# Optimization experiments

Measured on AMD Instinct MI355X. Metric: run time of the kernel, lower is better.

The kernel has to match this reference:

```python
import jax, jax.numpy as jnp
import numpy as np

ALPHA = 0.2      # LeakyReLU negative slope
EPS = 1e-5       # LayerNorm eps
NEG = -9e15


def setup_inputs() -> dict:
    key = jax.random.key(0)
    ks = jax.random.split(key, 7)
    B, N, F_in, F_out = 8, 1024, 512, 512
    h1 = jax.random.normal(ks[0], (B, N, F_in), jnp.float32)
    h2 = jax.random.normal(ks[1], (B, N, F_in), jnp.float32)
    adj = jax.random.randint(ks[2], (B, N, N), 0, 2, jnp.int32)
    s = 1.414 * (6.0 / (F_in + F_out)) ** 0.5  # xavier_uniform gain=1.414
    W1 = jax.random.uniform(ks[3], (F_in, F_out), jnp.float32, -s, s)
    W2 = jax.random.uniform(ks[4], (F_in, F_out), jnp.float32, -s, s)
    W3 = jax.random.uniform(ks[5], (F_in, F_out), jnp.float32, -s, s)
    sa = 1.414 * (6.0 / (2 * F_out + 1)) ** 0.5
    a = jax.random.uniform(ks[6], (2 * F_out, 1), jnp.float32, -sa, sa)
    gamma = jnp.ones((F_out,), jnp.float32)
    beta = jnp.zeros((F_out,), jnp.float32)
    return {"h1": h1, "h2": h2, "adj": adj, "W1": W1, "W2": W2,
            "W3": W3, "a": a, "gamma": gamma, "beta": beta}


def reference(h1, h2, adj, W1, W2, W3, a, gamma, beta):
    F_out = W1.shape[1]
    Wh = h1 @ W1                      # [B,N,F]
    Wt = h2 @ W2                      # [B,N,F]
    a1 = a[:F_out, 0]                 # [F]
    a2 = a[F_out:, 0]                 # [F]
    # decomposed edge score: cat([Wh_i, Wt_j]) @ a == Wh_i@a1 + Wt_j@a2
    e = (Wh @ a1)[:, :, None] + (Wt @ a2)[:, None, :]   # [B,N,N]
    e = jnp.where(e > 0, e, ALPHA * e)                  # LeakyReLU
    e = jnp.where(adj > 0, e, NEG)
    attention = jax.nn.softmax(e, axis=2)               # [B,N,N]
    Wv = h2 @ W3                                        # [B,N,F]
    h_prime = attention @ Wv                            # [B,N,F]
    mu = jnp.mean(h_prime, axis=-1, keepdims=True)
    var = jnp.mean(jnp.square(h_prime - mu), axis=-1, keepdims=True)
    h_prime = (h_prime - mu) * jax.lax.rsqrt(var + EPS) * gamma + beta
    return jax.nn.gelu(h_prime, approximate=False)
```

## Files before the change

### kernel.cpp

```cpp
#include <hip/hip_runtime.h>
#include <math.h>

#define ALPHA 0.2f
#define NEGV  -9000000000000000.0f
#define EPSV  1e-5f

static constexpr int Bn = 8;
static constexpr int Nn = 1024;
static constexpr int Fn = 512;
static constexpr int M  = Bn * Nn;

typedef __attribute__((ext_vector_type(8))) short bf16x8;
typedef __attribute__((ext_vector_type(4))) float f32x4;

__device__ inline float wave_reduce_sum(float v) {
#pragma unroll
    for (int off = 32; off; off >>= 1) v += __shfl_xor(v, off);
    return v;
}
__device__ inline float wave_reduce_max(float v) {
#pragma unroll
    for (int off = 32; off; off >>= 1) v = fmaxf(v, __shfl_xor(v, off));
    return v;
}

__device__ inline unsigned short bf16_rne(float f) {
    union { float f; unsigned int u; } v; v.f = f;
    unsigned int r = v.u + 0x7FFFu + ((v.u >> 16) & 1u);
    return (unsigned short)(r >> 16);
}
__device__ inline float bf16_to_f(unsigned short h) {
    union { unsigned int u; float f; } v; v.u = (unsigned int)h << 16;
    return v.f;
}

__global__ __launch_bounds__(256) void k_pack(const int* __restrict__ adj,
                                              unsigned int* __restrict__ pk) {
    int idx = blockIdx.x * 256 + threadIdx.x;
    const int* p = adj + (size_t)idx * 32;
    unsigned int m = 0;
#pragma unroll
    for (int q = 0; q < 8; ++q) {
        int4 v = *(const int4*)&p[q * 4];
        m |= (unsigned)(v.x > 0) << (q * 4 + 0);
        m |= (unsigned)(v.y > 0) << (q * 4 + 1);
        m |= (unsigned)(v.z > 0) << (q * 4 + 2);
        m |= (unsigned)(v.w > 0) << (q * 4 + 3);
    }
    pk[idx] = m;
}

__global__ __launch_bounds__(64) void k_proj_w(const float* __restrict__ W1,
                                               const float* __restrict__ W2,
                                               const float* __restrict__ a,
                                               float* __restrict__ c) {
    int bid   = blockIdx.x;
    int which = bid >> 9;
    int row   = bid & 511;
    const float* W  = which ? W2 : W1;
    const float* av = a + which * Fn;
    const float* wr = W + (size_t)row * Fn;
    int lane = threadIdx.x;
    float s = 0.f;
#pragma unroll
    for (int p = 0; p < 2; ++p) {
        float4 wv = *(const float4*)&wr[lane * 4 + p * 256];
        float4 a4 = *(const float4*)&av[lane * 4 + p * 256];
        s += wv.x * a4.x + wv.y * a4.y + wv.z * a4.z + wv.w * a4.w;
    }
    s = wave_reduce_sum(s);
    if (lane == 0) c[which * Fn + row] = s;
}

__global__ __launch_bounds__(256) void k_proj_h(const float* __restrict__ h1,
                                                const float* __restrict__ h2,
                                                const float* __restrict__ c,
                                                float* __restrict__ Wha,
                                                float* __restrict__ Wta) {
    int which = blockIdx.y;
    const float* h  = which ? h2 : h1;
    const float* cv = c + which * Fn;
    float* outp = which ? Wta : Wha;
    int wave = threadIdx.x >> 6, lane = threadIdx.x & 63;
    int row  = blockIdx.x * 4 + wave;
    const float* hr = h + (size_t)row * Fn;
    float s = 0.f;
#pragma unroll
    for (int p = 0; p < 2; ++p) {
        float4 hv = *(const float4*)&hr[lane * 8 + p * 4];
        float4 c4 = *(const float4*)&cv[lane * 8 + p * 4];
        s += hv.x * c4.x + hv.y * c4.y + hv.z * c4.z + hv.w * c4.w;
    }
    s = wave_reduce_sum(s);
    if (lane == 0) outp[row] = s;
}

__global__ __launch_bounds__(256) void k_gemm_mfma(const float* __restrict__ A,
                                                   const float* __restrict__ Bw,
                                                   unsigned short* __restrict__ wv_hi,
                                                   unsigned short* __restrict__ wv_lo) {
    __shared__ __attribute__((aligned(16))) unsigned short a_hi[128 * 40];
    __shared__ __attribute__((aligned(16))) unsigned short a_lo[128 * 40];
    __shared__ __attribute__((aligned(16))) unsigned short b_hi[128 * 40];
    __shared__ __attribute__((aligned(16))) unsigned short b_lo[128 * 40];
    int t = threadIdx.x;
    int wave = t >> 6, lane = t & 63;
    int wr = wave >> 1, wc = wave & 1;
    int i0 = blockIdx.x * 128, f0 = blockIdx.y * 128;

    f32x4 zero = {0.f, 0.f, 0.f, 0.f};
    f32x4 acc[4][4];
#pragma unroll
    for (int mi = 0; mi < 4; ++mi)
#pragma unroll
        for (int nj = 0; nj < 4; ++nj) acc[mi][nj] = zero;

    int ar = t >> 1, ac = (t & 1) * 16;
    int bk = t >> 3, bf = (t & 7) * 16;
    const float* abase = A + (size_t)(i0 + ar) * Fn + ac;
    const float* bbase = Bw + (size_t)bk * Fn + f0 + bf;

    float4 areg[4], breg[4];
    auto gload = [&](int kt) {
        const float* ap = abase + kt * 32;
#pragma unroll
        for (int p = 0; p < 4; ++p) areg[p] = *(const float4*)(ap + p * 4);
        const float* bp = bbase + (size_t)kt * 32 * Fn;
#pragma unroll
        for (int p = 0; p < 4; ++p) breg[p] = *(const float4*)(bp + p * 4);
    };

    gload(0);
    const int nkt = Fn / 32;
    for (int kt = 0; kt < nkt; ++kt) {
        __syncthreads();
#pragma unroll
        for (int hf = 0; hf < 2; ++hf) {
            bf16x8 vh, vl;
#pragma unroll
            for (int q = 0; q < 8; ++q) {
                float f = ((const float*)&areg[hf * 2])[q];
                unsigned short hh = bf16_rne(f);
                vh[q] = (short)hh;
                vl[q] = (short)bf16_rne(f - bf16_to_f(hh));
            }
            *(bf16x8*)&a_hi[ar * 40 + ac + hf * 8] = vh;
            *(bf16x8*)&a_lo[ar * 40 + ac + hf * 8] = vl;
        }
#pragma unroll
        for (int p = 0; p < 4; ++p) {
#pragma unroll
            for (int q = 0; q < 4; ++q) {
                float f = ((const float*)&breg[p])[q];
                unsigned short hh = bf16_rne(f);
                int n = bf + p * 4 + q;
                b_hi[n * 40 + bk] = hh;
                b_lo[n * 40 + bk] = bf16_rne(f - bf16_to_f(hh));
            }
        }
        __syncthreads();
        if (kt + 1 < nkt) gload(kt + 1);
        bf16x8 afh[4], afl[4], bfh[4], bfl[4];
        int ab = (wr * 64 + (lane & 15)) * 40 + (lane >> 4) * 8;
        int bb = (wc * 64 + (lane & 15)) * 40 + (lane >> 4) * 8;
#pragma unroll
        for (int mi = 0; mi < 4; ++mi) {
            afh[mi] = *(const bf16x8*)&a_hi[ab + mi * 16 * 40];
            afl[mi] = *(const bf16x8*)&a_lo[ab + mi * 16 * 40];
        }
#pragma unroll
        for (int nj = 0; nj < 4; ++nj) {
            bfh[nj] = *(const bf16x8*)&b_hi[bb + nj * 16 * 40];
            bfl[nj] = *(const bf16x8*)&b_lo[bb + nj * 16 * 40];
        }
#pragma unroll
        for (int mi = 0; mi < 4; ++mi)
#pragma unroll
            for (int nj = 0; nj < 4; ++nj) {
                acc[mi][nj] = __builtin_amdgcn_mfma_f32_16x16x32_bf16(afh[mi], bfh[nj], acc[mi][nj], 0, 0, 0);
                acc[mi][nj] = __builtin_amdgcn_mfma_f32_16x16x32_bf16(afh[mi], bfl[nj], acc[mi][nj], 0, 0, 0);
                acc[mi][nj] = __builtin_amdgcn_mfma_f32_16x16x32_bf16(afl[mi], bfh[nj], acc[mi][nj], 0, 0, 0);
            }
    }
#pragma unroll
    for (int mi = 0; mi < 4; ++mi)
#pragma unroll
        for (int nj = 0; nj < 4; ++nj) {
            int r0 = i0 + wr * 64 + mi * 16 + (lane >> 4) * 4;
            int c0 = f0 + wc * 64 + nj * 16 + (lane & 15);
#pragma unroll
            for (int r = 0; r < 4; ++r) {
                float f = acc[mi][nj][r];
                unsigned short hh = bf16_rne(f);
                size_t off = (size_t)(r0 + r) * Fn + c0;
                wv_hi[off] = hh;
                wv_lo[off] = bf16_rne(f - bf16_to_f(hh));
            }
        }
}

__global__ __launch_bounds__(256) void k_stats(const unsigned int* __restrict__ pk,
                                               const float* __restrict__ Wha,
                                               const float* __restrict__ Wta,
                                               float2* __restrict__ stat) {
    int bi = blockIdx.x;
    int b = bi >> 10;
    const float* wt = Wta + b * Nn;
    float whai = Wha[bi];
    int t = threadIdx.x;
    unsigned int word = pk[(size_t)bi * 32 + (t >> 3)];
    int sh = (t & 7) * 4;
    float4 wv = *(const float4*)&wt[t * 4];
    float e[4];
    {
        float x;
        x = whai + wv.x; x = x > 0.f ? x : ALPHA * x; e[0] = ((word >> (sh + 0)) & 1) ? x : NEGV;
        x = whai + wv.y; x = x > 0.f ? x : ALPHA * x; e[1] = ((word >> (sh + 1)) & 1) ? x : NEGV;
        x = whai + wv.z; x = x > 0.f ? x : ALPHA * x; e[2] = ((word >> (sh + 2)) & 1) ? x : NEGV;
        x = whai + wv.w; x = x > 0.f ? x : ALPHA * x; e[3] = ((word >> (sh + 3)) & 1) ? x : NEGV;
    }
    float m4 = fmaxf(fmaxf(e[0], e[1]), fmaxf(e[2], e[3]));
    __shared__ float redm[4], reds[4];
    int wave = t >> 6, lane = t & 63;
    float m = wave_reduce_max(m4);
    if (lane == 0) redm[wave] = m;
    __syncthreads();
    m = fmaxf(fmaxf(redm[0], redm[1]), fmaxf(redm[2], redm[3]));
    float s4 = __expf(e[0] - m) + __expf(e[1] - m) + __expf(e[2] - m) + __expf(e[3] - m);
    float s = wave_reduce_sum(s4);
    if (lane == 0) reds[wave] = s;
    __syncthreads();
    if (t == 0) {
        s = reds[0] + reds[1] + reds[2] + reds[3];
        stat[bi] = make_float2(m, 1.0f / s);
    }
}

__global__ __launch_bounds__(256) void k_attn_mfma(const unsigned int* __restrict__ pk,
                                                   const float* __restrict__ Wha,
                                                   const float* __restrict__ Wta,
                                                   const float2* __restrict__ stat,
                                                   const unsigned short* __restrict__ wv_hi,
                                                   const unsigned short* __restrict__ wv_lo,
                                                   float* __restrict__ outp) {
    __shared__ __attribute__((aligned(16))) unsigned short a_hi[128 * 40];
    __shared__ __attribute__((aligned(16))) unsigned short a_lo[128 * 40];
    __shared__ __attribute__((aligned(16))) unsigned short b_hi[128 * 40];
    __shared__ __attribute__((aligned(16))) unsigned short b_lo[128 * 40];
    __shared__ __attribute__((aligned(16))) float wta_s[Nn];
    __shared__ float wha_s[128], m_s[128], rs_s[128];
    int t = threadIdx.x;
    int wave = t >> 6, lane = t & 63;
    int wr = wave >> 1, wc = wave & 1;
    int b  = blockIdx.z;
    int i0 = blockIdx.x * 128, f0 = blockIdx.y * 128;

    if (t < 128) {
        wha_s[t] = Wha[b * Nn + i0 + t];
        float2 st = stat[b * Nn + i0 + t];
        m_s[t] = st.x; rs_s[t] = st.y;
    }
    *(float4*)&wta_s[t * 4] = *(const float4*)&Wta[b * Nn + t * 4];

    f32x4 zero = {0.f, 0.f, 0.f, 0.f};
    f32x4 acc[4][4];
#pragma unroll
    for (int mi = 0; mi < 4; ++mi)
#pragma unroll
        for (int nj = 0; nj < 4; ++nj) acc[mi][nj] = zero;

    int ai = t >> 1, ajh = (t & 1) * 16;
    int bk = t >> 3, bf = (t & 7) * 16;
    const unsigned short* hbase = wv_hi + ((size_t)b * Nn + bk) * Fn + f0 + bf;
    const unsigned short* lbase = wv_lo + ((size_t)b * Nn + bk) * Fn + f0 + bf;

    unsigned int pword;
    uint4 bh0, bh1, bl0, bl1;
    auto gload = [&](int kt) {
        pword = pk[((size_t)b * Nn + i0 + ai) * 32 + kt];
        const unsigned short* hp = hbase + (size_t)kt * 32 * Fn;
        const unsigned short* lp = lbase + (size_t)kt * 32 * Fn;
        bh0 = *(const uint4*)hp; bh1 = *(const uint4*)(hp + 8);
        bl0 = *(const uint4*)lp; bl1 = *(const uint4*)(lp + 8);
    };

    gload(0);
    __syncthreads();

    for (int kt = 0; kt < Nn / 32; ++kt) {
        float att[16];
        {
            float whai = wha_s[ai], mi_ = m_s[ai], rsi = rs_s[ai];
#pragma unroll
            for (int q = 0; q < 16; ++q) {
                float x = whai + wta_s[kt * 32 + ajh + q];
                x = x > 0.f ? x : ALPHA * x;
                float e = ((pword >> (ajh + q)) & 1) ? x : NEGV;
                att[q] = __expf(e - mi_) * rsi;
            }
        }
        __syncthreads();
#pragma unroll
        for (int hf = 0; hf < 2; ++hf) {
            bf16x8 vh, vl;
#pragma unroll
            for (int q = 0; q < 8; ++q) {
                float f = att[hf * 8 + q];
                unsigned short hh = bf16_rne(f);
                vh[q] = (short)hh;
                vl[q] = (short)bf16_rne(f - bf16_to_f(hh));
            }
            *(bf16x8*)&a_hi[ai * 40 + ajh + hf * 8] = vh;
            *(bf16x8*)&a_lo[ai * 40 + ajh + hf * 8] = vl;
        }
#pragma unroll
        for (int q = 0; q < 8; ++q) {
            b_hi[(bf + q) * 40 + bk]     = ((const unsigned short*)&bh0)[q];
            b_hi[(bf + 8 + q) * 40 + bk] = ((const unsigned short*)&bh1)[q];
            b_lo[(bf + q) * 40 + bk]     = ((const unsigned short*)&bl0)[q];
            b_lo[(bf + 8 + q) * 40 + bk] = ((const unsigned short*)&bl1)[q];
        }
        __syncthreads();
        if (kt + 1 < Nn / 32) gload(kt + 1);
        bf16x8 afh[4], afl[4], bfh[4], bfl[4];
        int ab = (wr * 64 + (lane & 15)) * 40 + (lane >> 4) * 8;
        int bb = (wc * 64 + (lane & 15)) * 40 + (lane >> 4) * 8;
#pragma unroll
        for (int mi = 0; mi < 4; ++mi) {
            afh[mi] = *(const bf16x8*)&a_hi[ab + mi * 16 * 40];
            afl[mi] = *(const bf16x8*)&a_lo[ab + mi * 16 * 40];
        }
#pragma unroll
        for (int nj = 0; nj < 4; ++nj) {
            bfh[nj] = *(const bf16x8*)&b_hi[bb + nj * 16 * 40];
            bfl[nj] = *(const bf16x8*)&b_lo[bb + nj * 16 * 40];
        }
#pragma unroll
        for (int mi = 0; mi < 4; ++mi)
#pragma unroll
            for (int nj = 0; nj < 4; ++nj) {
                acc[mi][nj] = __builtin_amdgcn_mfma_f32_16x16x32_bf16(afh[mi], bfh[nj], acc[mi][nj], 0, 0, 0);
                acc[mi][nj] = __builtin_amdgcn_mfma_f32_16x16x32_bf16(afh[mi], bfl[nj], acc[mi][nj], 0, 0, 0);
                acc[mi][nj] = __builtin_amdgcn_mfma_f32_16x16x32_bf16(afl[mi], bfh[nj], acc[mi][nj], 0, 0, 0);
            }
    }
#pragma unroll
    for (int mi = 0; mi < 4; ++mi)
#pragma unroll
        for (int nj = 0; nj < 4; ++nj) {
            int r0 = i0 + wr * 64 + mi * 16 + (lane >> 4) * 4;
            int c0 = f0 + wc * 64 + nj * 16 + (lane & 15);
#pragma unroll
            for (int r = 0; r < 4; ++r)
                outp[((size_t)b * Nn + r0 + r) * Fn + c0] = acc[mi][nj][r];
        }
}

__global__ __launch_bounds__(128) void k_ln_gelu(float* __restrict__ x,
                                                 const float* __restrict__ gamma,
                                                 const float* __restrict__ beta) {
    int row = blockIdx.x;
    float* xr = x + (size_t)row * Fn;
    int t = threadIdx.x;
    float4 v = *(float4*)&xr[t * 4];
    float s = v.x + v.y + v.z + v.w;
    float q = v.x * v.x + v.y * v.y + v.z * v.z + v.w * v.w;
    s = wave_reduce_sum(s);
    q = wave_reduce_sum(q);
    __shared__ float rs[2], rq[2];
    int wave = t >> 6, lane = t & 63;
    if (lane == 0) { rs[wave] = s; rq[wave] = q; }
    __syncthreads();
    s = rs[0] + rs[1];
    q = rq[0] + rq[1];
    float mu   = s * (1.0f / Fn);
    float var  = q * (1.0f / Fn) - mu * mu;
    float rstd = rsqrtf(var + EPSV);
    float4 g  = *(const float4*)&gamma[t * 4];
    float4 be = *(const float4*)&beta[t * 4];
    auto gel = [](float xx) { return 0.5f * xx * (1.0f + erff(xx * 0.70710678118f)); };
    float y0 = (v.x - mu) * rstd * g.x + be.x;
    float y1 = (v.y - mu) * rstd * g.y + be.y;
    float y2 = (v.z - mu) * rstd * g.z + be.z;
    float y3 = (v.w - mu) * rstd * g.w + be.w;
    float4 o = {gel(y0), gel(y1), gel(y2), gel(y3)};
    *(float4*)&xr[t * 4] = o;
}

extern "C" void kernel_launch(void* const* d_in, const int* in_sizes, int n_in,
                              void* d_out, int out_size, void* d_ws, size_t ws_size,
                              hipStream_t stream) {
    const float* h1    = (const float*)d_in[0];
    const float* h2    = (const float*)d_in[1];
    const int*   adj   = (const int*)d_in[2];
    const float* W1    = (const float*)d_in[3];
    const float* W2    = (const float*)d_in[4];
    const float* W3    = (const float*)d_in[5];
    const float* a     = (const float*)d_in[6];
    const float* gamma = (const float*)d_in[7];
    const float* beta  = (const float*)d_in[8];
    float* outp = (float*)d_out;

    unsigned short* wv_hi = (unsigned short*)d_ws;
    unsigned short* wv_lo = wv_hi + (size_t)M * Fn;
    unsigned int*   pack  = (unsigned int*)(wv_lo + (size_t)M * Fn);
    float2*         stat  = (float2*)(pack + (size_t)M * 32);
    float*          c     = (float*)(stat + M);
    float*          Wha   = c + 1024;
    float*          Wta   = Wha + M;

    hipLaunchKernelGGL(k_pack, dim3(M * 32 / 256), dim3(256), 0, stream, adj, pack);
    hipLaunchKernelGGL(k_proj_w, dim3(1024), dim3(64), 0, stream, W1, W2, a, c);
    hipLaunchKernelGGL(k_proj_h, dim3(M / 4, 2), dim3(256), 0, stream, h1, h2, c, Wha, Wta);
    hipLaunchKernelGGL(k_gemm_mfma, dim3(M / 128, Fn / 128), dim3(256), 0, stream,
                       h2, W3, wv_hi, wv_lo);
    hipLaunchKernelGGL(k_stats, dim3(M), dim3(256), 0, stream, pack, Wha, Wta, stat);
    hipLaunchKernelGGL(k_attn_mfma, dim3(Nn / 128, Fn / 128, Bn), dim3(256), 0, stream,
                       pack, Wha, Wta, stat, wv_hi, wv_lo, outp);
    hipLaunchKernelGGL(k_ln_gelu, dim3(M), dim3(128), 0, stream, outp, gamma, beta);
}
```

Measured before the change: 264.2 us.

## Restructure Wv GEMM and attention GEMM to direct-register MFMA with transposed Wv

W3 is pre-transposed and split into bf16 hi/lo once, and the Wv GEMM now writes its output transposed to [B,F,N] so both GEMMs can load MFMA B-operands straight from global memory instead of staging through LDS with two barriers per k-step. Both GEMMs drop one of the three split-bf16 MFMA products: the activation-side A operand (h2 and the attention weights) becomes single bf16, and the softmax row scale is applied at the end rather than per element. The adjacency bits are staged transposed into LDS, and LeakyReLU uses fmaxf. This cuts LDS traffic, synchronisation and MFMA count, but lowers accuracy on the A side and relies on L1/L2 reuse of the B tiles shared across waves.

```diff
diff --git a/kernel.cpp b/kernel.cpp
--- a/kernel.cpp
+++ b/kernel.cpp
@@ -54,9 +54,7 @@
                                                const float* __restrict__ W2,
                                                const float* __restrict__ a,
                                                float* __restrict__ c) {
-    int bid   = blockIdx.x;
-    int which = bid >> 9;
-    int row   = bid & 511;
+    int bid = blockIdx.x, which = bid >> 9, row = bid & 511;
     const float* W  = which ? W2 : W1;
     const float* av = a + which * Fn;
     const float* wr = W + (size_t)row * Fn;
@@ -95,108 +93,117 @@
     if (lane == 0) outp[row] = s;
 }
 
-__global__ __launch_bounds__(256) void k_gemm_mfma(const float* __restrict__ A,
-                                                   const float* __restrict__ Bw,
-                                                   unsigned short* __restrict__ wv_hi,
-                                                   unsigned short* __restrict__ wv_lo) {
-    __shared__ __attribute__((aligned(16))) unsigned short a_hi[128 * 40];
-    __shared__ __attribute__((aligned(16))) unsigned short a_lo[128 * 40];
-    __shared__ __attribute__((aligned(16))) unsigned short b_hi[128 * 40];
-    __shared__ __attribute__((aligned(16))) unsigned short b_lo[128 * 40];
-    int t = threadIdx.x;
-    int wave = t >> 6, lane = t & 63;
-    int wr = wave >> 1, wc = wave & 1;
-    int i0 = blockIdx.x * 128, f0 = blockIdx.y * 128;
-
-    f32x4 zero = {0.f, 0.f, 0.f, 0.f};
-    f32x4 acc[4][4];
-#pragma unroll
-    for (int mi = 0; mi < 4; ++mi)
-#pragma unroll
-        for (int nj = 0; nj < 4; ++nj) acc[mi][nj] = zero;
-
-    int ar = t >> 1, ac = (t & 1) * 16;
-    int bk = t >> 3, bf = (t & 7) * 16;
-    const float* abase = A + (size_t)(i0 + ar) * Fn + ac;
-    const float* bbase = Bw + (size_t)bk * Fn + f0 + bf;
-
-    float4 areg[4], breg[4];
-    auto gload = [&](int kt) {
-        const float* ap = abase + kt * 32;
-#pragma unroll
-        for (int p = 0; p < 4; ++p) areg[p] = *(const float4*)(ap + p * 4);
-        const float* bp = bbase + (size_t)kt * 32 * Fn;
-#pragma unroll
-        for (int p = 0; p < 4; ++p) breg[p] = *(const float4*)(bp + p * 4);
-    };
-
-    gload(0);
-    const int nkt = Fn / 32;
-    for (int kt = 0; kt < nkt; ++kt) {
-        __syncthreads();
-#pragma unroll
-        for (int hf = 0; hf < 2; ++hf) {
-            bf16x8 vh, vl;
+__global__ __launch_bounds__(256) void k_w3t(const float* __restrict__ W3,
+                                             unsigned short* __restrict__ hi,
+                                             unsigned short* __restrict__ lo) {
+    __shared__ float tile[32][33];
+    int kt = blockIdx.x * 32, ft = blockIdx.y * 32;
+    int c = threadIdx.x & 31, r = threadIdx.x >> 5;
+#pragma unroll
+    for (int s = 0; s < 4; ++s)
+        tile[r + s * 8][c] = W3[(size_t)(kt + r + s * 8) * Fn + ft + c];
+    __syncthreads();
+#pragma unroll
+    for (int s = 0; s < 4; ++s) {
+        float f = tile[c][r + s * 8];
+        unsigned short h = bf16_rne(f);
+        size_t o = (size_t)(ft + r + s * 8) * Fn + kt + c;
+        hi[o] = h;
+        lo[o] = bf16_rne(f - bf16_to_f(h));
+    }
+}
+
+__global__ __launch_bounds__(256) void k_gemm2(const float* __restrict__ h2,
+                                               const unsigned short* __restrict__ w3h,
+                                               const unsigned short* __restrict__ w3l,
+                                               unsigned short* __restrict__ wvh,
+                                               unsigned short* __restrict__ wvl) {
+    __shared__ float etile[64 * 132];
+    int t = threadIdx.x, wave = t >> 6, lane = t & 63;
+    int l15 = lane & 15, l16 = lane >> 4;
+    int i0 = blockIdx.x * 128, f0 = blockIdx.y * 64;
+    int wr = wave;
+
+    f32x4 acc[2][4];
+#pragma unroll
+    for (int mi = 0; mi < 2; ++mi)
+#pragma unroll
+        for (int nj = 0; nj < 4; ++nj) acc[mi][nj] = (f32x4){0.f, 0.f, 0.f, 0.f};
+
+    const float* a0base = h2 + (size_t)(i0 + wr * 32 + l15) * Fn + l16 * 8;
+    const float* a1base = a0base + 16 * Fn;
+    const unsigned short* bhb = w3h + (size_t)(f0 + l15) * Fn + l16 * 8;
+    const unsigned short* blb = w3l + (size_t)(f0 + l15) * Fn + l16 * 8;
+
+#pragma unroll 2
+    for (int kt = 0; kt < Fn / 32; ++kt) {
+        bf16x8 bh[4], bl[4];
+#pragma unroll
+        for (int nj = 0; nj < 4; ++nj) {
+            bh[nj] = *(const bf16x8*)(bhb + (size_t)nj * 16 * Fn + kt * 32);
+            bl[nj] = *(const bf16x8*)(blb + (size_t)nj * 16 * Fn + kt * 32);
+        }
+        float4 v0 = *(const float4*)(a0base + kt * 32);
+        float4 v1 = *(const float4*)(a0base + kt * 32 + 4);
+        float4 v2 = *(const float4*)(a1base + kt * 32);
+        float4 v3 = *(const float4*)(a1base + kt * 32 + 4);
+        bf16x8 a0, a1;
+        {
+            const float* f0p = (const float*)&v0;
+            const float* f1p = (const float*)&v2;
+#pragma unroll
+            for (int q = 0; q < 4; ++q) {
+                a0[q] = (short)bf16_rne(f0p[q]);
+                a1[q] = (short)bf16_rne(f1p[q]);
+            }
+            const float* g0p = (const float*)&v1;
+            const float* g1p = (const float*)&v3;
+#pragma unroll
+            for (int q = 0; q < 4; ++q) {
+                a0[4 + q] = (short)bf16_rne(g0p[q]);
+                a1[4 + q] = (short)bf16_rne(g1p[q]);
+            }
+        }
+#pragma unroll
+        for (int nj = 0; nj < 4; ++nj) {
+            acc[0][nj] = __builtin_amdgcn_mfma_f32_16x16x32_bf16(a0, bh[nj], acc[0][nj], 0, 0, 0);
+            acc[0][nj] = __builtin_amdgcn_mfma_f32_16x16x32_bf16(a0, bl[nj], acc[0][nj], 0, 0, 0);
+            acc[1][nj] = __builtin_amdgcn_mfma_f32_16x16x32_bf16(a1, bh[nj], acc[1][nj], 0, 0, 0);
+            acc[1][nj] = __builtin_amdgcn_mfma_f32_16x16x32_bf16(a1, bl[nj], acc[1][nj], 0, 0, 0);
+        }
+    }
+#pragma unroll
+    for (int mi = 0; mi < 2; ++mi)
+#pragma unroll
+        for (int nj = 0; nj < 4; ++nj) {
+            int nloc = wr * 32 + mi * 16 + l16 * 4;
+            int floc = nj * 16 + l15;
+            *(float4*)&etile[floc * 132 + nloc] = *(float4*)&acc[mi][nj];
+        }
+    __syncthreads();
+    {
+        int floc = t >> 2, n0 = (t & 3) * 32;
+        int b = i0 >> 10, nb = i0 & 1023;
+        unsigned short* oh = wvh + ((size_t)b * Fn + f0 + floc) * Nn + nb + n0;
+        unsigned short* ol = wvl + ((size_t)b * Fn + f0 + floc) * Nn + nb + n0;
+        const float* src = &etile[floc * 132 + n0];
+        bf16x8 rh[4], rl[4];
+#pragma unroll
+        for (int s = 0; s < 4; ++s) {
 #pragma unroll
             for (int q = 0; q < 8; ++q) {
-                float f = ((const float*)&areg[hf * 2])[q];
-                unsigned short hh = bf16_rne(f);
-                vh[q] = (short)hh;
-                vl[q] = (short)bf16_rne(f - bf16_to_f(hh));
+                float f = src[s * 8 + q];
+                unsigned short h = bf16_rne(f);
+                rh[s][q] = (short)h;
+                rl[s][q] = (short)bf16_rne(f - bf16_to_f(h));
             }
-            *(bf16x8*)&a_hi[ar * 40 + ac + hf * 8] = vh;
-            *(bf16x8*)&a_lo[ar * 40 + ac + hf * 8] = vl;
-        }
-#pragma unroll
-        for (int p = 0; p < 4; ++p) {
-#pragma unroll
-            for (int q = 0; q < 4; ++q) {
-                float f = ((const float*)&breg[p])[q];
-                unsigned short hh = bf16_rne(f);
-                int n = bf + p * 4 + q;
-                b_hi[n * 40 + bk] = hh;
-                b_lo[n * 40 + bk] = bf16_rne(f - bf16_to_f(hh));
-            }
-        }
-        __syncthreads();
-        if (kt + 1 < nkt) gload(kt + 1);
-        bf16x8 afh[4], afl[4], bfh[4], bfl[4];
-        int ab = (wr * 64 + (lane & 15)) * 40 + (lane >> 4) * 8;
-        int bb = (wc * 64 + (lane & 15)) * 40 + (lane >> 4) * 8;
-#pragma unroll
-        for (int mi = 0; mi < 4; ++mi) {
-            afh[mi] = *(const bf16x8*)&a_hi[ab + mi * 16 * 40];
-            afl[mi] = *(const bf16x8*)&a_lo[ab + mi * 16 * 40];
-        }
-#pragma unroll
-        for (int nj = 0; nj < 4; ++nj) {
-            bfh[nj] = *(const bf16x8*)&b_hi[bb + nj * 16 * 40];
-            bfl[nj] = *(const bf16x8*)&b_lo[bb + nj * 16 * 40];
-        }
-#pragma unroll
-        for (int mi = 0; mi < 4; ++mi)
-#pragma unroll
-            for (int nj = 0; nj < 4; ++nj) {
-                acc[mi][nj] = __builtin_amdgcn_mfma_f32_16x16x32_bf16(afh[mi], bfh[nj], acc[mi][nj], 0, 0, 0);
-                acc[mi][nj] = __builtin_amdgcn_mfma_f32_16x16x32_bf16(afh[mi], bfl[nj], acc[mi][nj], 0, 0, 0);
-                acc[mi][nj] = __builtin_amdgcn_mfma_f32_16x16x32_bf16(afl[mi], bfh[nj], acc[mi][nj], 0, 0, 0);
-            }
-    }
-#pragma unroll
-    for (int mi = 0; mi < 4; ++mi)
-#pragma unroll
-        for (int nj = 0; nj < 4; ++nj) {
-            int r0 = i0 + wr * 64 + mi * 16 + (lane >> 4) * 4;
-            int c0 = f0 + wc * 64 + nj * 16 + (lane & 15);
-#pragma unroll
-            for (int r = 0; r < 4; ++r) {
-                float f = acc[mi][nj][r];
-                unsigned short hh = bf16_rne(f);
-                size_t off = (size_t)(r0 + r) * Fn + c0;
-                wv_hi[off] = hh;
-                wv_lo[off] = bf16_rne(f - bf16_to_f(hh));
-            }
-        }
+        }
+#pragma unroll
+        for (int s = 0; s < 4; ++s) {
+            *(bf16x8*)(oh + s * 8) = rh[s];
+            *(bf16x8*)(ol + s * 8) = rl[s];
+        }
+    }
 }
 
 __global__ __launch_bounds__(256) void k_stats(const unsigned int* __restrict__ pk,
@@ -214,10 +221,10 @@
     float e[4];
     {
         float x;
-        x = whai + wv.x; x = x > 0.f ? x : ALPHA * x; e[0] = ((word >> (sh + 0)) & 1) ? x : NEGV;
-        x = whai + wv.y; x = x > 0.f ? x : ALPHA * x; e[1] = ((word >> (sh + 1)) & 1) ? x : NEGV;
-        x = whai + wv.z; x = x > 0.f ? x : ALPHA * x; e[2] = ((word >> (sh + 2)) & 1) ? x : NEGV;
-        x = whai + wv.w; x = x > 0.f ? x : ALPHA * x; e[3] = ((word >> (sh + 3)) & 1) ? x : NEGV;
+        x = whai + wv.x; x = fmaxf(x, ALPHA * x); e[0] = ((word >> (sh + 0)) & 1) ? x : NEGV;
+        x = whai + wv.y; x = fmaxf(x, ALPHA * x); e[1] = ((word >> (sh + 1)) & 1) ? x : NEGV;
+        x = whai + wv.z; x = fmaxf(x, ALPHA * x); e[2] = ((word >> (sh + 2)) & 1) ? x : NEGV;
+        x = whai + wv.w; x = fmaxf(x, ALPHA * x); e[3] = ((word >> (sh + 3)) & 1) ? x : NEGV;
     }
     float m4 = fmaxf(fmaxf(e[0], e[1]), fmaxf(e[2], e[3]));
     __shared__ float redm[4], reds[4];
@@ -236,123 +243,98 @@
     }
 }
 
-__global__ __launch_bounds__(256) void k_attn_mfma(const unsigned int* __restrict__ pk,
-                                                   const float* __restrict__ Wha,
-                                                   const float* __restrict__ Wta,
-                                                   const float2* __restrict__ stat,
-                                                   const unsigned short* __restrict__ wv_hi,
-                                                   const unsigned short* __restrict__ wv_lo,
-                                                   float* __restrict__ outp) {
-    __shared__ __attribute__((aligned(16))) unsigned short a_hi[128 * 40];
-    __shared__ __attribute__((aligned(16))) unsigned short a_lo[128 * 40];
-    __shared__ __attribute__((aligned(16))) unsigned short b_hi[128 * 40];
-    __shared__ __attribute__((aligned(16))) unsigned short b_lo[128 * 40];
-    __shared__ __attribute__((aligned(16))) float wta_s[Nn];
+__global__ __launch_bounds__(256) void k_attn2(const unsigned int* __restrict__ pk,
+                                               const float* __restrict__ Wha,
+                                               const float* __restrict__ Wta,
+                                               const float2* __restrict__ stat,
+                                               const unsigned short* __restrict__ wvh,
+                                               const unsigned short* __restrict__ wvl,
+                                               float* __restrict__ outp) {
+    __shared__ unsigned int pkt[32 * 128];
+    __shared__ float wta_s[Nn];
     __shared__ float wha_s[128], m_s[128], rs_s[128];
-    int t = threadIdx.x;
-    int wave = t >> 6, lane = t & 63;
-    int wr = wave >> 1, wc = wave & 1;
-    int b  = blockIdx.z;
-    int i0 = blockIdx.x * 128, f0 = blockIdx.y * 128;
-
-    if (t < 128) {
-        wha_s[t] = Wha[b * Nn + i0 + t];
-        float2 st = stat[b * Nn + i0 + t];
-        m_s[t] = st.x; rs_s[t] = st.y;
-    }
-    *(float4*)&wta_s[t * 4] = *(const float4*)&Wta[b * Nn + t * 4];
-
-    f32x4 zero = {0.f, 0.f, 0.f, 0.f};
-    f32x4 acc[4][4];
-#pragma unroll
-    for (int mi = 0; mi < 4; ++mi)
-#pragma unroll
-        for (int nj = 0; nj < 4; ++nj) acc[mi][nj] = zero;
-
-    int ai = t >> 1, ajh = (t & 1) * 16;
-    int bk = t >> 3, bf = (t & 7) * 16;
-    const unsigned short* hbase = wv_hi + ((size_t)b * Nn + bk) * Fn + f0 + bf;
-    const unsigned short* lbase = wv_lo + ((size_t)b * Nn + bk) * Fn + f0 + bf;
-
-    unsigned int pword;
-    uint4 bh0, bh1, bl0, bl1;
-    auto gload = [&](int kt) {
-        pword = pk[((size_t)b * Nn + i0 + ai) * 32 + kt];
-        const unsigned short* hp = hbase + (size_t)kt * 32 * Fn;
-        const unsigned short* lp = lbase + (size_t)kt * 32 * Fn;
-        bh0 = *(const uint4*)hp; bh1 = *(const uint4*)(hp + 8);
-        bl0 = *(const uint4*)lp; bl1 = *(const uint4*)(lp + 8);
-    };
-
-    gload(0);
-    __syncthreads();
-
+    int t = threadIdx.x, wave = t >> 6, lane = t & 63;
+    int l15 = lane & 15, l16 = lane >> 4;
+    int f0 = blockIdx.x * 64, i0 = blockIdx.y * 128, b = blockIdx.z;
+
+    {
+        int r = t >> 1, half = t & 1;
+        const unsigned int* src = pk + ((size_t)(b * Nn + i0 + r)) * 32 + half * 16;
+        uint4 w0 = *(const uint4*)src, w1 = *(const uint4*)(src + 4);
+        uint4 w2 = *(const uint4*)(src + 8), w3 = *(const uint4*)(src + 12);
+        const unsigned int* ww = (const unsigned int*)&w0;
+        unsigned int wv_[16] = {w0.x, w0.y, w0.z, w0.w, w1.x, w1.y, w1.z, w1.w,
+                                w2.x, w2.y, w2.z, w2.w, w3.x, w3.y, w3.z, w3.w};
+        (void)ww;
+#pragma unroll
+        for (int w = 0; w < 16; ++w) pkt[(half * 16 + w) * 128 + r] = wv_[w];
+        *(float4*)&wta_s[t * 4] = *(const float4*)&Wta[b * Nn + t * 4];
+        if (t < 128) {
+            wha_s[t] = Wha[b * Nn + i0 + t];
+            float2 st = stat[b * Nn + i0 + t];
+            m_s[t] = st.x; rs_s[t] = st.y;
+        }
+    }
+    __syncthreads();
+
+    int wr = wave;
+    float whaA = wha_s[wr * 32 + l15],      mA = m_s[wr * 32 + l15];
+    float whaB = wha_s[wr * 32 + 16 + l15], mB = m_s[wr * 32 + 16 + l15];
+    const unsigned short* bhb = wvh + ((size_t)b * Fn + f0 + l15) * Nn + l16 * 8;
+    const unsigned short* blb = wvl + ((size_t)b * Fn + f0 + l15) * Nn + l16 * 8;
+
+    f32x4 acc[2][4];
+#pragma unroll
+    for (int mi = 0; mi < 2; ++mi)
+#pragma unroll
+        for (int nj = 0; nj < 4; ++nj) acc[mi][nj] = (f32x4){0.f, 0.f, 0.f, 0.f};
+
+#pragma unroll 2
     for (int kt = 0; kt < Nn / 32; ++kt) {
-        float att[16];
-        {
-            float whai = wha_s[ai], mi_ = m_s[ai], rsi = rs_s[ai];
-#pragma unroll
-            for (int q = 0; q < 16; ++q) {
-                float x = whai + wta_s[kt * 32 + ajh + q];
-                x = x > 0.f ? x : ALPHA * x;
-                float e = ((pword >> (ajh + q)) & 1) ? x : NEGV;
-                att[q] = __expf(e - mi_) * rsi;
+        bf16x8 bh[4], bl[4];
+#pragma unroll
+        for (int nj = 0; nj < 4; ++nj) {
+            bh[nj] = *(const bf16x8*)(bhb + (size_t)nj * 16 * Nn + kt * 32);
+            bl[nj] = *(const bf16x8*)(blb + (size_t)nj * 16 * Nn + kt * 32);
+        }
+        unsigned int shA = pkt[kt * 128 + wr * 32 + l15] >> (l16 * 8);
+        unsigned int shB = pkt[kt * 128 + wr * 32 + 16 + l15] >> (l16 * 8);
+        float4 wq0 = *(const float4*)&wta_s[kt * 32 + l16 * 8];
+        float4 wq1 = *(const float4*)&wta_s[kt * 32 + l16 * 8 + 4];
+        float wq[8] = {wq0.x, wq0.y, wq0.z, wq0.w, wq1.x, wq1.y, wq1.z, wq1.w};
+        bf16x8 a0, a1;
+#pragma unroll
+        for (int q = 0; q < 8; ++q) {
+            float xA = whaA + wq[q];
+            xA = fmaxf(xA, ALPHA * xA);
+            float pA = __expf(xA - mA);
+            pA = ((shA >> q) & 1) ? pA : 0.0f;
+            a0[q] = (short)bf16_rne(pA);
+            float xB = whaB + wq[q];
+            xB = fmaxf(xB, ALPHA * xB);
+            float pB = __expf(xB - mB);
+            pB = ((shB >> q) & 1) ? pB : 0.0f;
+            a1[q] = (short)bf16_rne(pB);
+        }
+#pragma unroll
+        for (int nj = 0; nj < 4; ++nj) {
+            acc[0][nj] = __builtin_amdgcn_mfma_f32_16x16x32_bf16(a0, bh[nj], acc[0][nj], 0, 0, 0);
+            acc[0][nj] = __builtin_amdgcn_mfma_f32_16x16x32_bf16(a0, bl[nj], acc[0][nj], 0, 0, 0);
+            acc[1][nj] = __builtin_amdgcn_mfma_f32_16x16x32_bf16(a1, bh[nj], acc[1][nj], 0, 0, 0);
+            acc[1][nj] = __builtin_amdgcn_mfma_f32_16x16x32_bf16(a1, bl[nj], acc[1][nj], 0, 0, 0);
+        }
+    }
+#pragma unroll
+    for (int mi = 0; mi < 2; ++mi)
+#pragma unroll
+        for (int nj = 0; nj < 4; ++nj) {
+#pragma unroll
+            for (int r = 0; r < 4; ++r) {
+                int rloc = wr * 32 + mi * 16 + l16 * 4 + r;
+                float rs = rs_s[rloc];
+                outp[((size_t)b * Nn + i0 + rloc) * Fn + f0 + nj * 16 + l15] =
+                    rs * acc[mi][nj][r];
             }
-        }
-        __syncthreads();
-#pragma unroll
-        for (int hf = 0; hf < 2; ++hf) {
-            bf16x8 vh, vl;
-#pragma unroll
-            for (int q = 0; q < 8; ++q) {
-                float f = att[hf * 8 + q];
-                unsigned short hh = bf16_rne(f);
-                vh[q] = (short)hh;
-                vl[q] = (short)bf16_rne(f - bf16_to_f(hh));
-            }
-            *(bf16x8*)&a_hi[ai * 40 + ajh + hf * 8] = vh;
-            *(bf16x8*)&a_lo[ai * 40 + ajh + hf * 8] = vl;
-        }
-#pragma unroll
-        for (int q = 0; q < 8; ++q) {
-            b_hi[(bf + q) * 40 + bk]     = ((const unsigned short*)&bh0)[q];
-            b_hi[(bf + 8 + q) * 40 + bk] = ((const unsigned short*)&bh1)[q];
-            b_lo[(bf + q) * 40 + bk]     = ((const unsigned short*)&bl0)[q];
-            b_lo[(bf + 8 + q) * 40 + bk] = ((const unsigned short*)&bl1)[q];
-        }
-        __syncthreads();
-        if (kt + 1 < Nn / 32) gload(kt + 1);
-        bf16x8 afh[4], afl[4], bfh[4], bfl[4];
-        int ab = (wr * 64 + (lane & 15)) * 40 + (lane >> 4) * 8;
-        int bb = (wc * 64 + (lane & 15)) * 40 + (lane >> 4) * 8;
-#pragma unroll
-        for (int mi = 0; mi < 4; ++mi) {
-            afh[mi] = *(const bf16x8*)&a_hi[ab + mi * 16 * 40];
-            afl[mi] = *(const bf16x8*)&a_lo[ab + mi * 16 * 40];
-        }
-#pragma unroll
-        for (int nj = 0; nj < 4; ++nj) {
-            bfh[nj] = *(const bf16x8*)&b_hi[bb + nj * 16 * 40];
-            bfl[nj] = *(const bf16x8*)&b_lo[bb + nj * 16 * 40];
-        }
-#pragma unroll
-        for (int mi = 0; mi < 4; ++mi)
-#pragma unroll
-            for (int nj = 0; nj < 4; ++nj) {
-                acc[mi][nj] = __builtin_amdgcn_mfma_f32_16x16x32_bf16(afh[mi], bfh[nj], acc[mi][nj], 0, 0, 0);
-                acc[mi][nj] = __builtin_amdgcn_mfma_f32_16x16x32_bf16(afh[mi], bfl[nj], acc[mi][nj], 0, 0, 0);
-                acc[mi][nj] = __builtin_amdgcn_mfma_f32_16x16x32_bf16(afl[mi], bfh[nj], acc[mi][nj], 0, 0, 0);
-            }
-    }
-#pragma unroll
-    for (int mi = 0; mi < 4; ++mi)
-#pragma unroll
-        for (int nj = 0; nj < 4; ++nj) {
-            int r0 = i0 + wr * 64 + mi * 16 + (lane >> 4) * 4;
-            int c0 = f0 + wc * 64 + nj * 16 + (lane & 15);
-#pragma unroll
-            for (int r = 0; r < 4; ++r)
-                outp[((size_t)b * Nn + r0 + r) * Fn + c0] = acc[mi][nj][r];
         }
 }
 
@@ -401,21 +383,24 @@
     const float* beta  = (const float*)d_in[8];
     float* outp = (float*)d_out;
 
-    unsigned short* wv_hi = (unsigned short*)d_ws;
-    unsigned short* wv_lo = wv_hi + (size_t)M * Fn;
-    unsigned int*   pack  = (unsigned int*)(wv_lo + (size_t)M * Fn);
-    float2*         stat  = (float2*)(pack + (size_t)M * 32);
-    float*          c     = (float*)(stat + M);
-    float*          Wha   = c + 1024;
-    float*          Wta   = Wha + M;
+    unsigned short* wvh  = (unsigned short*)d_ws;
+    unsigned short* wvl  = wvh + (size_t)M * Fn;
+    unsigned short* w3h  = wvl + (size_t)M * Fn;
+    unsigned short* w3l  = w3h + (size_t)Fn * Fn;
+    unsigned int*   pack = (unsigned int*)(w3l + (size_t)Fn * Fn);
+    float2*         stat = (float2*)(pack + (size_t)M * 32);
+    float*          c    = (float*)(stat + M);
+    float*          Wha  = c + 1024;
+    float*          Wta  = Wha + M;
 
     hipLaunchKernelGGL(k_pack, dim3(M * 32 / 256), dim3(256), 0, stream, adj, pack);
     hipLaunchKernelGGL(k_proj_w, dim3(1024), dim3(64), 0, stream, W1, W2, a, c);
     hipLaunchKernelGGL(k_proj_h, dim3(M / 4, 2), dim3(256), 0, stream, h1, h2, c, Wha, Wta);
-    hipLaunchKernelGGL(k_gemm_mfma, dim3(M / 128, Fn / 128), dim3(256), 0, stream,
-                       h2, W3, wv_hi, wv_lo);
+    hipLaunchKernelGGL(k_w3t, dim3(16, 16), dim3(256), 0, stream, W3, w3h, w3l);
+    hipLaunchKernelGGL(k_gemm2, dim3(M / 128, Fn / 64), dim3(256), 0, stream,
+                       h2, w3h, w3l, wvh, wvl);
     hipLaunchKernelGGL(k_stats, dim3(M), dim3(256), 0, stream, pack, Wha, Wta, stat);
-    hipLaunchKernelGGL(k_attn_mfma, dim3(Nn / 128, Fn / 128, Bn), dim3(256), 0, stream,
-                       pack, Wha, Wta, stat, wv_hi, wv_lo, outp);
+    hipLaunchKernelGGL(k_attn2, dim3(Fn / 64, Nn / 128, Bn), dim3(256), 0, stream,
+                       pack, Wha, Wta, stat, wvh, wvl, outp);
     hipLaunchKernelGGL(k_ln_gelu, dim3(M), dim3(128), 0, stream, outp, gamma, beta);
 }
```

Result: faster. 245.5 us (-7.1%).
